# Performance work log

Hardware: AMD Instinct MI355X
Metric: run time of the kernel (lower is better)

Reference implementation:

```python
import jax, jax.numpy as jnp
import numpy as np

# Static configuration (from init_kwargs)
SPLIT_SEC = (128, 320, 320)   # (n_nucl_species..., n_up, n_dn)
N = sum(SPLIT_SEC)            # 768 particles
N_NUCL = sum(SPLIT_SEC[:-2])  # 128
N_DN = SPLIT_SEC[-1]          # 320
SINGLE = 256
PAIR = 64
D_FEAT = SINGLE + len(SPLIT_SEC) * PAIR + len(SPLIT_SEC) * SINGLE  # 1216
SQRT2 = 1.4142135623730951
GELU_RESCALE = 1.7128586      # fvmc rescaled-gelu constant (unit output variance)

_SPLIT_IDX = np.cumsum(SPLIT_SEC)[:-1]

def _pair_type():
    pt = np.zeros((N, N), np.int32)
    sn, se = slice(0, N_NUCL), slice(N_NUCL, N)
    su = slice(N_NUCL, N_NUCL + SPLIT_SEC[-2])
    sd = slice(N_NUCL + SPLIT_SEC[-2], N)
    pt[sn, se] = pt[se, sn] = 1
    pt[su, su] = pt[sd, sd] = 2
    pt[su, sd] = pt[sd, su] = 3
    return pt

PAIR_TYPE = _pair_type()  # static int mask, values in {0,1,2,3}

def actv(x):
    # parse_activation('gelu', rescale=True)
    return jax.nn.gelu(x) * GELU_RESCALE

def residual(x, y):
    # adaptive_residual with rescale=True (shapes always match here)
    return (x + y) / SQRT2

def aggregate_features(h1, h2):
    # per-section mean of h1 over particles -> (n_sec, d1), tiled to (N, n_sec, d1)
    h1_mean = jnp.stack([s.mean(axis=0) for s in jnp.split(h1, _SPLIT_IDX, axis=0)], axis=0)
    h1_mean = jnp.tile(h1_mean[None], (N, 1, 1))
    # per-section mean of h2 over axis 1 -> (N, n_sec, d2)
    h2_mean = jnp.stack([s.mean(axis=1) for s in jnp.split(h2, _SPLIT_IDX, axis=1)], axis=-2)
    # spin symmetry: swap the last two (up/dn) mean channels for the dn rows
    h1_sw = jnp.stack([h1_mean[-N_DN:, -1], h1_mean[-N_DN:, -2]], axis=1)
    h1_mean = h1_mean.at[-N_DN:, -2:].set(h1_sw)
    h2_sw = jnp.stack([h2_mean[-N_DN:, -1], h2_mean[-N_DN:, -2]], axis=1)
    h2_mean = h2_mean.at[-N_DN:, -2:].set(h2_sw)
    return jnp.concatenate([h1, h2_mean.reshape(N, -1), h1_mean.reshape(N, -1)], axis=-1)

def setup_inputs() -> dict:
    key = jax.random.key(0)
    ks = jax.random.split(key, 5)
    sc = lambda fan_in: 1.0 / np.sqrt(fan_in)  # lecun-normal-ish scale
    return {
        "h1": jax.random.normal(ks[0], (N, SINGLE), jnp.float32),
        "h2": jax.random.normal(ks[1], (N, N, PAIR), jnp.float32),
        "W1n": jax.random.normal(ks[2], (D_FEAT, SINGLE), jnp.float32) * sc(D_FEAT),
        "b1n": jnp.zeros((SINGLE,), jnp.float32),
        "W1e": jax.random.normal(ks[3], (D_FEAT, SINGLE), jnp.float32) * sc(D_FEAT),
        "b1e": jnp.zeros((SINGLE,), jnp.float32),
        "W2": jax.random.normal(ks[4], (4, PAIR, PAIR), jnp.float32) * sc(PAIR),
        "b2": jnp.zeros((4, PAIR), jnp.float32),
    }

def reference(h1, h2, W1n, b1n, W1e, b1e, W2, b2):
    feats = aggregate_features(h1, h2)  # (N, D_FEAT)
    # h1 update: separate Dense for nuclei vs electrons
    h1_new = jnp.concatenate([
        feats[:N_NUCL] @ W1n + b1n,
        feats[N_NUCL:] @ W1e + b1e,
    ], axis=0)
    h1_out = residual(h1, actv(h1_new))
    # h2 update: per pair-type Dense, masked scatter back (4 static types)
    pt = jnp.asarray(PAIR_TYPE)
    h2_new = jnp.zeros((N, N, PAIR), h2.dtype)
    for p in range(4):
        mask = (pt == p)[..., None]
        h2_new = h2_new + mask * (jnp.einsum('nmd,de->nme', h2, W2[p]) + b2[p])
    h2_out = residual(h2, actv(h2_new))
    return h1_out, h2_out
```

## Files before the change

### kernel.cpp

```cpp
#include <hip/hip_runtime.h>


#define H1OUT_ELEMS (768 * 256)

typedef short short8 __attribute__((ext_vector_type(8)));
typedef float f32x4 __attribute__((ext_vector_type(4)));

__device__ __forceinline__ unsigned short f2bf(float f) {
    unsigned u = __builtin_bit_cast(unsigned, f);
    unsigned r = u + 0x7fffu + ((u >> 16) & 1u);
    return (unsigned short)(r >> 16);
}

__device__ __forceinline__ float gelu_res(float x, float hv) {
    float x2 = x * x;
    float z = x * fmaf(-0.1029432196f, x2, -2.3025850930f);
    float e = __builtin_amdgcn_exp2f(z);
    float r = __builtin_amdgcn_rcpf(1.f + e);
    return fmaf(x * r, 1.2111740f, hv * 0.70710678f);
}

__global__ __launch_bounds__(256) void k_h2pre(
    const float* __restrict__ h2, const float* __restrict__ W2,
    const float* __restrict__ b2, const float* __restrict__ h1,
    const float* __restrict__ W1n, const float* __restrict__ W1e,
    float* __restrict__ out2, float* __restrict__ part2,
    float* __restrict__ part1, unsigned short* __restrict__ WT) {
    __shared__ union SM {
        struct {
            float ot[64][68];
            float red[16][68];
        } g;
        float tile2[64][33];
    } sm;

    int b = blockIdx.x;
    const int t = threadIdx.x;

    if (b < 12) {
        float s = 0.f;
        #pragma unroll 8
        for (int r = 0; r < 64; ++r) s += h1[(size_t)(b * 64 + r) * 256 + t];
        part1[b * 256 + t] = s;
        return;
    }
    if (b < 316) {
        int idx = b - 12;
        int mtx = idx / 152;
        int r2  = idx % 152;
        int k0 = (r2 >> 3) * 64, e0 = (r2 & 7) * 32;
        const float* W = mtx ? W1e : W1n;
        #pragma unroll
        for (int i = 0; i < 8; ++i) {
            int j = i * 256 + t;
            int kr = j >> 5, ec = j & 31;
            sm.tile2[kr][ec] = W[(size_t)(k0 + kr) * 256 + e0 + ec];
        }
        __syncthreads();
        int er = t >> 3, k8 = (t & 7) * 8;
        short8 o;
        #pragma unroll
        for (int j = 0; j < 8; ++j) o[j] = (short)f2bf(sm.tile2[k8 + j][er]);
        *reinterpret_cast<short8*>(
            &WT[((size_t)mtx * 256 + e0 + er) * 1216 + k0 + k8]) = o;
        return;
    }

    b -= 316;
    const int ct = b % 12;
    const int n  = b / 12;
    const int m0 = ct * 64;

    const int rs = (n < 128) ? 0 : ((n < 448) ? 1 : 2);
    const int cs = (ct < 2) ? 0 : ((ct < 7) ? 1 : 2);
    int p;
    if (rs == 0)      p = (cs == 0) ? 0 : 1;
    else if (rs == 1) p = (cs == 0) ? 1 : ((cs == 1) ? 2 : 3);
    else              p = (cs == 0) ? 1 : ((cs == 1) ? 3 : 2);

    const float* src = h2 + ((size_t)n * 768 + m0) * 64;
    const int lane = t & 63;
    const int wv = t >> 6;
    const int wm = wv >> 1, we = wv & 1;
    const int lr = lane & 15, lk = lane >> 4;

    f32x4 hv[4];
    #pragma unroll
    for (int i = 0; i < 4; ++i)
        hv[i] = *reinterpret_cast<const f32x4*>(src + i * 1024 + t * 4);

    const float* arow = src + (wm * 32 + lr) * 64 + lk * 8;
    float4 af[2][2][2];
    #pragma unroll
    for (int fm = 0; fm < 2; ++fm)
        #pragma unroll
        for (int kh = 0; kh < 2; ++kh) {
            const float* pp = arow + fm * 1024 + kh * 32;
            af[fm][kh][0] = *reinterpret_cast<const float4*>(pp);
            af[fm][kh][1] = *reinterpret_cast<const float4*>(pp + 4);
        }

    const float* wp = W2 + p * 4096 + we * 32 + lr;
    short8 bF[2][2];
    #pragma unroll
    for (int fe = 0; fe < 2; ++fe)
        #pragma unroll
        for (int kh = 0; kh < 2; ++kh) {
            const float* q = wp + fe * 16 + (kh * 32 + lk * 8) * 64;
            short8 o;
            #pragma unroll
            for (int j = 0; j < 8; ++j) o[j] = (short)f2bf(q[j * 64]);
            bF[fe][kh] = o;
        }

    short8 aF[2][2];
    #pragma unroll
    for (int fm = 0; fm < 2; ++fm)
        #pragma unroll
        for (int kh = 0; kh < 2; ++kh) {
            short8 o;
            o[0] = (short)f2bf(af[fm][kh][0].x);
            o[1] = (short)f2bf(af[fm][kh][0].y);
            o[2] = (short)f2bf(af[fm][kh][0].z);
            o[3] = (short)f2bf(af[fm][kh][0].w);
            o[4] = (short)f2bf(af[fm][kh][1].x);
            o[5] = (short)f2bf(af[fm][kh][1].y);
            o[6] = (short)f2bf(af[fm][kh][1].z);
            o[7] = (short)f2bf(af[fm][kh][1].w);
            aF[fm][kh] = o;
        }

    {
        f32x4 s;
        s[0] = hv[0][0] + hv[1][0] + hv[2][0] + hv[3][0];
        s[1] = hv[0][1] + hv[1][1] + hv[2][1] + hv[3][1];
        s[2] = hv[0][2] + hv[1][2] + hv[2][2] + hv[3][2];
        s[3] = hv[0][3] + hv[1][3] + hv[2][3] + hv[3][3];
        *reinterpret_cast<f32x4*>(&sm.g.red[t >> 4][(t & 15) * 4]) = s;
    }

    f32x4 acc[2][2] = {};
    #pragma unroll
    for (int kh = 0; kh < 2; ++kh)
        #pragma unroll
        for (int fm = 0; fm < 2; ++fm)
            #pragma unroll
            for (int fe = 0; fe < 2; ++fe)
                acc[fm][fe] = __builtin_amdgcn_mfma_f32_16x16x32_bf16(
                    aF[fm][kh], bF[fe][kh], acc[fm][fe], 0, 0, 0);

    #pragma unroll
    for (int fm = 0; fm < 2; ++fm) {
        #pragma unroll
        for (int fe = 0; fe < 2; ++fe) {
            int e = we * 32 + fe * 16 + lr;
            float bias = b2[p * 64 + e];
            #pragma unroll
            for (int r = 0; r < 4; ++r) {
                int m = wm * 32 + fm * 16 + lk * 4 + r;
                sm.g.ot[m][e] = acc[fm][fe][r] + bias;
            }
        }
    }
    __syncthreads();

    if (t < 64) {
        float s = 0.f;
        #pragma unroll
        for (int r = 0; r < 16; ++r) s += sm.g.red[r][t];
        part2[((size_t)n * 12 + ct) * 64 + t] = s;
    }

    float* dst = out2 + ((size_t)n * 768 + m0) * 64;
    #pragma unroll
    for (int i = 0; i < 4; ++i) {
        int flat = i * 1024 + t * 4;
        int m = flat >> 6, e = flat & 63;
        f32x4 x4 = *reinterpret_cast<const f32x4*>(&sm.g.ot[m][e]);
        f32x4 o;
        o[0] = gelu_res(x4[0], hv[i][0]);
        o[1] = gelu_res(x4[1], hv[i][1]);
        o[2] = gelu_res(x4[2], hv[i][2]);
        o[3] = gelu_res(x4[3], hv[i][3]);
        __builtin_nontemporal_store(o, reinterpret_cast<f32x4*>(dst + flat));
    }
}

__global__ __launch_bounds__(256) void k_h1f(
    const float* __restrict__ h1, const unsigned short* __restrict__ WT,
    const float* __restrict__ part2, const float* __restrict__ part1,
    const float* __restrict__ b1n, const float* __restrict__ b1e,
    float* __restrict__ out1) {
    __shared__ unsigned short FL[16][1224];

    const int n0 = blockIdx.x * 16;
    const int half = blockIdx.y;
    const int t = threadIdx.x;
    const bool dn = (n0 >= 448);
    const bool nucl = (n0 < 128);

    #pragma unroll
    for (int i = 0; i < 16; ++i) {
        int idx = i * 256 + t;
        int r = idx >> 8, c = idx & 255;
        FL[r][c] = f2bf(h1[(size_t)(n0 + r) * 256 + c]);
    }
    #pragma unroll
    for (int i = 0; i < 12; ++i) {
        int idx = i * 256 + t;
        int r = idx / 192, c = idx % 192;
        int sec = c >> 6, d = c & 63;
        int s2 = (dn && sec >= 1) ? (3 - sec) : sec;
        const float* pr = part2 + (size_t)(n0 + r) * 768;
        float s;
        if (s2 == 0) {
            s = (pr[d] + pr[64 + d]) * (1.f / 128.f);
        } else {
            int q0 = (s2 == 1) ? 2 : 7;
            s = 0.f;
            #pragma unroll
            for (int q = 0; q < 5; ++q) s += pr[(q0 + q) * 64 + d];
            s *= (1.f / 320.f);
        }
        FL[r][256 + c] = f2bf(s);
    }
    #pragma unroll
    for (int i = 0; i < 3; ++i) {
        int j = i * 256 + t;
        int sec = j >> 8, e2 = j & 255;
        int s2 = (dn && sec >= 1) ? (3 - sec) : sec;
        float s;
        if (s2 == 0) {
            s = (part1[e2] + part1[256 + e2]) * (1.f / 128.f);
        } else {
            int q0 = (s2 == 1) ? 2 : 7;
            s = 0.f;
            #pragma unroll
            for (int q = 0; q < 5; ++q) s += part1[(q0 + q) * 256 + e2];
            s *= (1.f / 320.f);
        }
        unsigned short bv = f2bf(s);
        #pragma unroll
        for (int r = 0; r < 16; ++r) FL[r][448 + j] = bv;
    }
    __syncthreads();

    const int w = t >> 6, lane = t & 63;
    const int lr = lane & 15, lk = lane >> 4;
    const int e0 = half * 128 + w * 32;
    const unsigned short* BT = WT + (nucl ? 0 : (size_t)256 * 1216);
    const unsigned short* br0 = BT + (size_t)(e0 + lr) * 1216 + lk * 8;
    const unsigned short* br1 = br0 + (size_t)16 * 1216;
    const unsigned short* ar = &FL[lr][lk * 8];

    f32x4 acc0 = {}, acc1 = {};
    #pragma unroll 2
    for (int k = 0; k < 1216; k += 32) {
        short8 aF = *reinterpret_cast<const short8*>(ar + k);
        short8 b0 = *reinterpret_cast<const short8*>(br0 + k);
        short8 b1 = *reinterpret_cast<const short8*>(br1 + k);
        acc0 = __builtin_amdgcn_mfma_f32_16x16x32_bf16(b0, aF, acc0, 0, 0, 0);
        acc1 = __builtin_amdgcn_mfma_f32_16x16x32_bf16(b1, aF, acc1, 0, 0, 0);
    }

    const float* bb = nucl ? b1n : b1e;
    const int m = n0 + lr;
    #pragma unroll
    for (int j = 0; j < 2; ++j) {
        const f32x4 a = j ? acc1 : acc0;
        int e = e0 + j * 16 + lk * 4;
        f32x4 bias4 = *reinterpret_cast<const f32x4*>(bb + e);
        f32x4 hv = *reinterpret_cast<const f32x4*>(h1 + (size_t)m * 256 + e);
        f32x4 o;
        o[0] = gelu_res(a[0] + bias4[0], hv[0]);
        o[1] = gelu_res(a[1] + bias4[1], hv[1]);
        o[2] = gelu_res(a[2] + bias4[2], hv[2]);
        o[3] = gelu_res(a[3] + bias4[3], hv[3]);
        *reinterpret_cast<f32x4*>(out1 + (size_t)m * 256 + e) = o;
    }
}

extern "C" void kernel_launch(void* const* d_in, const int* in_sizes, int n_in,
                              void* d_out, int out_size, void* d_ws, size_t ws_size,
                              hipStream_t stream) {
    const float* h1  = (const float*)d_in[0];
    const float* h2  = (const float*)d_in[1];
    const float* W1n = (const float*)d_in[2];
    const float* b1n = (const float*)d_in[3];
    const float* W1e = (const float*)d_in[4];
    const float* b1e = (const float*)d_in[5];
    const float* W2  = (const float*)d_in[6];
    const float* b2  = (const float*)d_in[7];

    float* out1 = (float*)d_out;
    float* out2 = out1 + H1OUT_ELEMS;

    float* part2 = (float*)d_ws;
    float* part1 = part2 + 768 * 12 * 64;
    unsigned short* WT = (unsigned short*)(part1 + 12 * 256);

    k_h2pre<<<dim3(316 + 12 * 768), 256, 0, stream>>>(
        h2, W2, b2, h1, W1n, W1e, out2, part2, part1, WT);
    k_h1f<<<dim3(48, 2), 256, 0, stream>>>(h1, WT, part2, part1, b1n, b1e, out1);
}
```

Before: 78.20 us.

## Give each wave its own 16 rows of the h2 tile and drop the full-block barrier

The h2 pair-update blocks now split work so each wave owns 16 contiguous rows and all 64 output columns, instead of a 2x2 split of rows by columns. The GELU epilogue reads only that wave's own shared-memory slice, so the transpose-through-LDS stage no longer needs a block-wide barrier. The only remaining barrier sits before the column-sum reduction and is issued early. The aim is to remove synchronisation stalls and shrink live registers. In exchange, every wave now loads and converts the full 64x64 W2 weight slice itself, which adds redundant global loads and bf16 conversions per wave.

```diff
diff --git a/kernel.cpp b/kernel.cpp
--- a/kernel.cpp
+++ b/kernel.cpp
@@ -28,8 +28,8 @@
     float* __restrict__ part1, unsigned short* __restrict__ WT) {
     __shared__ union SM {
         struct {
-            float ot[64][68];
-            float red[16][68];
+            float ot[4][16][68];
+            float red[4][4][64];
         } g;
         float tile2[64][33];
     } sm;
@@ -80,55 +80,23 @@
 
     const float* src = h2 + ((size_t)n * 768 + m0) * 64;
     const int lane = t & 63;
-    const int wv = t >> 6;
-    const int wm = wv >> 1, we = wv & 1;
+    const int w = t >> 6;
     const int lr = lane & 15, lk = lane >> 4;
-
+    const int r0 = w * 16;
+
+    const float* hbase = src + r0 * 64;
     f32x4 hv[4];
     #pragma unroll
     for (int i = 0; i < 4; ++i)
-        hv[i] = *reinterpret_cast<const f32x4*>(src + i * 1024 + t * 4);
-
-    const float* arow = src + (wm * 32 + lr) * 64 + lk * 8;
-    float4 af[2][2][2];
-    #pragma unroll
-    for (int fm = 0; fm < 2; ++fm)
-        #pragma unroll
-        for (int kh = 0; kh < 2; ++kh) {
-            const float* pp = arow + fm * 1024 + kh * 32;
-            af[fm][kh][0] = *reinterpret_cast<const float4*>(pp);
-            af[fm][kh][1] = *reinterpret_cast<const float4*>(pp + 4);
-        }
-
-    const float* wp = W2 + p * 4096 + we * 32 + lr;
-    short8 bF[2][2];
-    #pragma unroll
-    for (int fe = 0; fe < 2; ++fe)
-        #pragma unroll
-        for (int kh = 0; kh < 2; ++kh) {
-            const float* q = wp + fe * 16 + (kh * 32 + lk * 8) * 64;
-            short8 o;
-            #pragma unroll
-            for (int j = 0; j < 8; ++j) o[j] = (short)f2bf(q[j * 64]);
-            bF[fe][kh] = o;
-        }
-
-    short8 aF[2][2];
-    #pragma unroll
-    for (int fm = 0; fm < 2; ++fm)
-        #pragma unroll
-        for (int kh = 0; kh < 2; ++kh) {
-            short8 o;
-            o[0] = (short)f2bf(af[fm][kh][0].x);
-            o[1] = (short)f2bf(af[fm][kh][0].y);
-            o[2] = (short)f2bf(af[fm][kh][0].z);
-            o[3] = (short)f2bf(af[fm][kh][0].w);
-            o[4] = (short)f2bf(af[fm][kh][1].x);
-            o[5] = (short)f2bf(af[fm][kh][1].y);
-            o[6] = (short)f2bf(af[fm][kh][1].z);
-            o[7] = (short)f2bf(af[fm][kh][1].w);
-            aF[fm][kh] = o;
-        }
+        hv[i] = *reinterpret_cast<const f32x4*>(hbase + i * 256 + lane * 4);
+
+    const float* arow = src + (r0 + lr) * 64 + lk * 8;
+    float4 af[2][2];
+    #pragma unroll
+    for (int kh = 0; kh < 2; ++kh) {
+        af[kh][0] = *reinterpret_cast<const float4*>(arow + kh * 32);
+        af[kh][1] = *reinterpret_cast<const float4*>(arow + kh * 32 + 4);
+    }
 
     {
         f32x4 s;
@@ -136,53 +104,66 @@
         s[1] = hv[0][1] + hv[1][1] + hv[2][1] + hv[3][1];
         s[2] = hv[0][2] + hv[1][2] + hv[2][2] + hv[3][2];
         s[3] = hv[0][3] + hv[1][3] + hv[2][3] + hv[3][3];
-        *reinterpret_cast<f32x4*>(&sm.g.red[t >> 4][(t & 15) * 4]) = s;
-    }
-
-    f32x4 acc[2][2] = {};
-    #pragma unroll
-    for (int kh = 0; kh < 2; ++kh)
-        #pragma unroll
-        for (int fm = 0; fm < 2; ++fm)
-            #pragma unroll
-            for (int fe = 0; fe < 2; ++fe)
-                acc[fm][fe] = __builtin_amdgcn_mfma_f32_16x16x32_bf16(
-                    aF[fm][kh], bF[fe][kh], acc[fm][fe], 0, 0, 0);
-
-    #pragma unroll
-    for (int fm = 0; fm < 2; ++fm) {
-        #pragma unroll
-        for (int fe = 0; fe < 2; ++fe) {
-            int e = we * 32 + fe * 16 + lr;
-            float bias = b2[p * 64 + e];
-            #pragma unroll
-            for (int r = 0; r < 4; ++r) {
-                int m = wm * 32 + fm * 16 + lk * 4 + r;
-                sm.g.ot[m][e] = acc[fm][fe][r] + bias;
-            }
-        }
-    }
-    __syncthreads();
+        *reinterpret_cast<f32x4*>(&sm.g.red[w][lane >> 4][(lane & 15) * 4]) = s;
+    }
+
+    asm volatile("s_waitcnt lgkmcnt(0)" ::: "memory");
+    __builtin_amdgcn_s_barrier();
+    asm volatile("" ::: "memory");
 
     if (t < 64) {
         float s = 0.f;
         #pragma unroll
-        for (int r = 0; r < 16; ++r) s += sm.g.red[r][t];
+        for (int q = 0; q < 16; ++q) s += sm.g.red[q >> 2][q & 3][t];
         part2[((size_t)n * 12 + ct) * 64 + t] = s;
     }
 
-    float* dst = out2 + ((size_t)n * 768 + m0) * 64;
+    short8 aF[2];
+    #pragma unroll
+    for (int kh = 0; kh < 2; ++kh) {
+        short8 o;
+        o[0] = (short)f2bf(af[kh][0].x);
+        o[1] = (short)f2bf(af[kh][0].y);
+        o[2] = (short)f2bf(af[kh][0].z);
+        o[3] = (short)f2bf(af[kh][0].w);
+        o[4] = (short)f2bf(af[kh][1].x);
+        o[5] = (short)f2bf(af[kh][1].y);
+        o[6] = (short)f2bf(af[kh][1].z);
+        o[7] = (short)f2bf(af[kh][1].w);
+        aF[kh] = o;
+    }
+
+    const float* wp = W2 + p * 4096;
+    #pragma unroll
+    for (int fe = 0; fe < 4; ++fe) {
+        const float* q = wp + fe * 16 + lr;
+        short8 b0, b1;
+        #pragma unroll
+        for (int j = 0; j < 8; ++j) {
+            b0[j] = (short)f2bf(q[(lk * 8 + j) * 64]);
+            b1[j] = (short)f2bf(q[(32 + lk * 8 + j) * 64]);
+        }
+        f32x4 acc = {};
+        acc = __builtin_amdgcn_mfma_f32_16x16x32_bf16(aF[0], b0, acc, 0, 0, 0);
+        acc = __builtin_amdgcn_mfma_f32_16x16x32_bf16(aF[1], b1, acc, 0, 0, 0);
+        float bias = b2[p * 64 + fe * 16 + lr];
+        #pragma unroll
+        for (int r = 0; r < 4; ++r)
+            sm.g.ot[w][lk * 4 + r][fe * 16 + lr] = acc[r] + bias;
+    }
+
+    float* dst = out2 + ((size_t)n * 768 + m0 + r0) * 64;
     #pragma unroll
     for (int i = 0; i < 4; ++i) {
-        int flat = i * 1024 + t * 4;
-        int m = flat >> 6, e = flat & 63;
-        f32x4 x4 = *reinterpret_cast<const f32x4*>(&sm.g.ot[m][e]);
+        int row = i * 4 + (lane >> 4), col = (lane & 15) * 4;
+        f32x4 x4 = *reinterpret_cast<const f32x4*>(&sm.g.ot[w][row][col]);
         f32x4 o;
         o[0] = gelu_res(x4[0], hv[i][0]);
         o[1] = gelu_res(x4[1], hv[i][1]);
         o[2] = gelu_res(x4[2], hv[i][2]);
         o[3] = gelu_res(x4[3], hv[i][3]);
-        __builtin_nontemporal_store(o, reinterpret_cast<f32x4*>(dst + flat));
+        __builtin_nontemporal_store(
+            o, reinterpret_cast<f32x4*>(dst + i * 256 + lane * 4));
     }
 }
 
```

New measurement: 73.87 us. 5.5% less time.
